# Performance work log

Hardware: AMD Instinct MI355X
Metric: run time of the kernel (lower is better)

Reference implementation:

```python
import jax, jax.numpy as jnp
import numpy as np

NUM_GROUPS = 4
NUM_HEADS = 4
EPS = 1e-6

def group_norm(x, scale, bias):
    # x: [B, C, L]
    b, c, l = x.shape
    g = NUM_GROUPS
    xg = x.reshape(b, g, (c // g) * l)
    mean = xg.mean(axis=-1, keepdims=True)
    var = xg.var(axis=-1, keepdims=True)
    xg = (xg - mean) * jax.lax.rsqrt(var + EPS)
    xn = xg.reshape(b, c, l)
    return xn * scale[None, :, None] + bias[None, :, None]

def conv1x1(x, w, b):
    # x: [B, C_in, L], w: [C_out, C_in], b: [C_out]
    return jnp.einsum('oc,bcl->bol', w, x) + b[None, :, None]

def setup_inputs() -> dict:
    key = jax.random.key(0)
    ks = jax.random.split(key, 11)
    B, C, L = 8, 512, 2048
    x = jax.random.normal(ks[0], (B, C, L), dtype=jnp.float32)
    s = 1.0 / np.sqrt(C)
    return {
        'x': x,
        'gn_scale': jnp.ones((C,), jnp.float32),
        'gn_bias': jnp.zeros((C,), jnp.float32),
        'wq': jax.random.normal(ks[1], (C, C), jnp.float32) * s,
        'bq': jnp.zeros((C,), jnp.float32),
        'wk': jax.random.normal(ks[2], (C, C), jnp.float32) * s,
        'bk': jnp.zeros((C,), jnp.float32),
        'wv': jax.random.normal(ks[3], (C, C), jnp.float32) * s,
        'bv': jnp.zeros((C,), jnp.float32),
        'wo': jax.random.normal(ks[4], (C, C), jnp.float32) * s,
        'bo': jnp.zeros((C,), jnp.float32),
    }

def reference(x, gn_scale, gn_bias, wq, bq, wk, bk, wv, bv, wo, bo):
    b, c, l = x.shape
    nh = NUM_HEADS
    hd = c // nh
    h_ = group_norm(x, gn_scale, gn_bias)
    q = conv1x1(h_, wq, bq).reshape(b, nh, hd, l)
    k = conv1x1(h_, wk, bk).reshape(b, nh, hd, l)
    v = conv1x1(h_, wv, bv).reshape(b, nh, hd, l)
    # scores: [b, nh, l(query), l(key)]
    w_ = jnp.einsum('bhdq,bhdk->bhqk', q, k) * (hd ** -0.5)
    w_ = jax.nn.softmax(w_, axis=-1)
    # attn: [b, nh, l(query), hd]
    attn = jnp.einsum('bhqk,bhdk->bhqd', w_, v)
    attn = attn.transpose(0, 1, 3, 2).reshape(b, c, l)
    out = conv1x1(attn, wo, bo)
    return x + out
```

## Files before the change

kernel.cpp:

```cpp
#include <hip/hip_runtime.h>


typedef unsigned short u16;
typedef unsigned int   u32;
typedef unsigned long long u64;
typedef __attribute__((ext_vector_type(8)))  short          bf16x8;
typedef __attribute__((ext_vector_type(4)))  float          f32x4;
typedef __attribute__((ext_vector_type(16))) float          f32x16;
typedef __attribute__((ext_vector_type(4)))  unsigned int   u32x4;
typedef __attribute__((ext_vector_type(8)))  unsigned short u16x8;

#define MFMA16(a, b, c) __builtin_amdgcn_mfma_f32_16x16x32_bf16((a), (b), (c), 0, 0, 0)
#define MFMA32(a, b, c) __builtin_amdgcn_mfma_f32_32x32x16_bf16((a), (b), (c), 0, 0, 0)

#define WAIT_VM8        16248
#define WAIT_LGKM0      49279
#define BARRIER() __builtin_amdgcn_s_barrier()

__device__ __forceinline__ u16 f2bf(float f) {
    union { float f; unsigned int i; } cv;
    cv.f = f;
    unsigned int u = cv.i;
    u += 0x7fffu + ((u >> 16) & 1);
    return (u16)(u >> 16);
}
__device__ __forceinline__ u32 fbits(float f) {
    union { float f; unsigned int i; } cv; cv.f = f; return cv.i;
}

__device__ __forceinline__ u32 cvtpk_bf16(float lo, float hi) {
    u32 d;
    asm("v_cvt_pk_bf16_f32 %0, %1, %2" : "=v"(d) : "v"(lo), "v"(hi));
    return d;
}
__device__ __forceinline__ void permswap(u32& a, u32& b) {
    asm("v_permlane32_swap_b32 %0, %1" : "+v"(a), "+v"(b));
}

__device__ __forceinline__ void async16(const u16* g, u16* l) {
    __builtin_amdgcn_global_load_lds(
        (const __attribute__((address_space(1))) unsigned int*)g,
        (__attribute__((address_space(3))) unsigned int*)l, 16, 0, 0);
}

#define BATCH 8
#define CCH   512
#define LEN   2048
#define NGRP  4
#define NHEAD 4
#define HD    128
#define GSIZE (128 * 2048)

__global__ __launch_bounds__(256) void prep_k(const float* __restrict__ x,
                                              float* __restrict__ stats,
                                              const float* __restrict__ w0,
                                              const float* __restrict__ w1,
                                              const float* __restrict__ w2,
                                              const float* __restrict__ w3,
                                              u16* __restrict__ dst) {
    const int bid = blockIdx.x;
    if (bid < 256) {
        const int grp   = bid >> 3;
        const int chunk = bid & 7;
        const int b = grp >> 2, g = grp & 3;
        const float* base = x + ((size_t)(b * CCH + g * 128 + chunk * 16)) * LEN;

        float s = 0.f, ss = 0.f;
        for (int i = 0; i < 32; ++i) {
            int cid = threadIdx.x + i * 256;
            f32x4 dv = *(const f32x4*)(base + (size_t)cid * 4);
            for (int u = 0; u < 4; ++u) { s += dv[u]; ss += dv[u] * dv[u]; }
        }
        for (int m = 1; m < 64; m <<= 1) {
            s  += __shfl_xor(s,  m, 64);
            ss += __shfl_xor(ss, m, 64);
        }
        __shared__ float red[8];
        int wid = threadIdx.x >> 6, lane = threadIdx.x & 63;
        if (lane == 0) { red[wid * 2] = s; red[wid * 2 + 1] = ss; }
        __syncthreads();
        if (threadIdx.x == 0) {
            float ts  = red[0] + red[2] + red[4] + red[6];
            float tss = red[1] + red[3] + red[5] + red[7];
            atomicAdd(&stats[grp * 2],     ts);
            atomicAdd(&stats[grp * 2 + 1], tss);
        }
    } else {
        const int wb = bid - 256;
        const int mat = wb >> 7, chunk = wb & 127;
        const float* src = (mat == 0) ? w0 : (mat == 1) ? w1 : (mat == 2) ? w2 : w3;
        const size_t base = (size_t)chunk * 2048 + (size_t)threadIdx.x * 8;
        f32x4 a = *(const f32x4*)(src + base);
        f32x4 b2 = *(const f32x4*)(src + base + 4);
        u16x8 o;
        for (int u = 0; u < 4; ++u) { o[u] = f2bf(a[u]); o[u + 4] = f2bf(b2[u]); }
        *(u16x8*)(dst + (size_t)mat * 262144 + base) = o;
    }
}

__global__ __launch_bounds__(256) void gn_apply_k(const float* __restrict__ x,
                                                  const float* __restrict__ gns,
                                                  const float* __restrict__ gnb,
                                                  const float* __restrict__ stats,
                                                  u16* __restrict__ hT) {
    __shared__ u16 Ts[64 * 72];
    const int b = blockIdx.z, c0 = blockIdx.y * 64, l0 = blockIdx.x * 64;
    const int g = c0 >> 7;
    const int tid = threadIdx.x;

    float sum   = stats[(b * NGRP + g) * 2];
    float sumsq = stats[(b * NGRP + g) * 2 + 1];
    const float invN = 1.f / (float)GSIZE;
    float mean = sum * invN;
    float var  = sumsq * invN - mean * mean;
    float rstd = rsqrtf(var + 1e-6f);

    for (int i = 0; i < 4; ++i) {
        int cid = tid + i * 256;
        int row = cid >> 4, c4 = cid & 15;
        int c = c0 + row;
        float sc = gns[c] * rstd;
        float bi = gnb[c] - mean * sc;
        f32x4 dv = *(const f32x4*)(x + ((size_t)(b * CCH + c)) * LEN + l0 + c4 * 4);
        for (int u = 0; u < 4; ++u)
            Ts[row * 72 + c4 * 4 + u] = f2bf(dv[u] * sc + bi);
    }
    __syncthreads();
    for (int i = 0; i < 2; ++i) {
        int cid = tid + i * 256;
        int lrow = cid >> 3, c8 = cid & 7;
        u16x8 ov;
        for (int u = 0; u < 8; ++u) ov[u] = Ts[(c8 * 8 + u) * 72 + lrow];
        *(u16x8*)(hT + ((size_t)b * LEN + l0 + lrow) * CCH + c0 + c8 * 8) = ov;
    }
}

__global__ __launch_bounds__(256, 2) void gemm01_k(const u16* __restrict__ hT,
                                                   const u16* __restrict__ wq_bf,
                                                   const u16* __restrict__ wk_bf,
                                                   const u16* __restrict__ wv_bf,
                                                   const float* __restrict__ bq,
                                                   const float* __restrict__ bk,
                                                   const float* __restrict__ bv,
                                                   u16* __restrict__ qT,
                                                   u16* __restrict__ kT,
                                                   u16* __restrict__ vbuf) {
    __shared__ u16 As[2][128 * 64];
    __shared__ u16 Bs[2][128 * 64];
    const int bid = blockIdx.x;
    const bool mode0 = (bid < 1024);
    int b, m0, n0;
    const u16 *Arow, *Brow;
    if (mode0) {
        b = bid >> 7; m0 = ((bid >> 3) & 15) * 128; n0 = (bid & 7) * 128;
        Arow = hT + ((size_t)b * LEN + m0) * 512;
        Brow = (n0 < 512) ? (wq_bf + (size_t)n0 * 512)
                          : (wk_bf + (size_t)(n0 - 512) * 512);
    } else {
        int bid2 = bid - 1024;
        b = bid2 >> 6; m0 = ((bid2 >> 4) & 3) * 128; n0 = (bid2 & 15) * 128;
        Arow = wv_bf + (size_t)m0 * 512;
        Brow = hT + ((size_t)b * LEN + n0) * 512;
    }

    const int tid = threadIdx.x;
    const int lane = tid & 63, wid = tid >> 6;
    const int quad = lane >> 4, l15 = lane & 15;
    const int wm = (wid & 1) * 64, wn = (wid >> 1) * 64;

    f32x4 acc[4][4] = {};
    const int srl = lane >> 3, scl = lane & 7;

#pragma unroll
    for (int i = 0; i < 4; ++i) {
        int rloc = wid * 32 + i * 8 + srl;
        int lc = scl ^ (rloc & 7);
        async16(Arow + (size_t)rloc * 512 + lc * 8, &As[0][(wid * 32 + i * 8) * 64]);
        async16(Brow + (size_t)rloc * 512 + lc * 8, &Bs[0][(wid * 32 + i * 8) * 64]);
    }
    __syncthreads();

    for (int kk = 0; kk < 8; ++kk) {
        const int p = kk & 1;
        if (kk < 7) {
            const int k0n = (kk + 1) * 64;
#pragma unroll
            for (int i = 0; i < 4; ++i) {
                int rloc = wid * 32 + i * 8 + srl;
                int lc = scl ^ (rloc & 7);
                async16(Arow + (size_t)rloc * 512 + k0n + lc * 8,
                        &As[1 - p][(wid * 32 + i * 8) * 64]);
                async16(Brow + (size_t)rloc * 512 + k0n + lc * 8,
                        &Bs[1 - p][(wid * 32 + i * 8) * 64]);
            }
        }
#pragma unroll
        for (int ks = 0; ks < 2; ++ks) {
            bf16x8 af[4], bfr[4];
            for (int t = 0; t < 4; ++t) {
                int ra = wm + t * 16 + l15, rb = wn + t * 16 + l15;
                af[t]  = *(const bf16x8*)(&As[p][ra * 64 + (((ks * 4 + quad) ^ (ra & 7))) * 8]);
                bfr[t] = *(const bf16x8*)(&Bs[p][rb * 64 + (((ks * 4 + quad) ^ (rb & 7))) * 8]);
            }
            for (int mt = 0; mt < 4; ++mt)
                for (int nt = 0; nt < 4; ++nt)
                    acc[mt][nt] = MFMA16(af[mt], bfr[nt], acc[mt][nt]);
        }
        __syncthreads();
    }

    if (mode0) {
        const int col0 = (n0 < 512) ? n0 : n0 - 512;
        const float* biasp = ((n0 < 512) ? bq : bk) + col0;
        u16* outp = (n0 < 512) ? qT : kT;
        for (int nt = 0; nt < 4; ++nt) {
            int nl = wn + nt * 16 + l15;
            float bv_ = biasp[nl];
            for (int mt = 0; mt < 4; ++mt)
                for (int r = 0; r < 4; ++r) {
                    int ml = wm + mt * 16 + quad * 4 + r;
                    size_t idx = ((size_t)b * LEN + m0 + ml) * 512 + col0 + nl;
                    outp[idx] = f2bf(acc[mt][nt][r] + bv_);
                }
        }
    } else {
        for (int mt = 0; mt < 4; ++mt)
            for (int r = 0; r < 4; ++r) {
                int ml = wm + mt * 16 + quad * 4 + r;
                float bv_ = bv[m0 + ml];
                for (int nt = 0; nt < 4; ++nt) {
                    int nl = wn + nt * 16 + l15;
                    size_t idx = ((size_t)(b * 512 + m0 + ml)) * LEN + n0 + nl;
                    vbuf[idx] = f2bf(acc[mt][nt][r] + bv_);
                }
            }
    }
}

__global__ __launch_bounds__(256, 2) void gemm2_k(const u16* __restrict__ A0,
                                                  const u16* __restrict__ B0,
                                                  const float* __restrict__ bias0,
                                                  const float* __restrict__ resid,
                                                  float* __restrict__ out0) {
    __shared__ u16 As[2][128 * 64];
    __shared__ u16 Bs[2][128 * 64];
    const int b  = blockIdx.z;
    const int n0 = blockIdx.x * 128;
    const int m0 = blockIdx.y * 128;
    const int tid = threadIdx.x;
    const int lane = tid & 63, wid = tid >> 6;
    const int quad = lane >> 4, l15 = lane & 15;
    const int wm = (wid & 1) * 64, wn = (wid >> 1) * 64;

    const u16* Arow = A0 + (size_t)m0 * 512;
    const u16* Brow = B0 + ((size_t)b * LEN + n0) * 512;

    f32x4 acc[4][4] = {};
    const int srl = lane >> 3, scl = lane & 7;

#pragma unroll
    for (int i = 0; i < 4; ++i) {
        int rloc = wid * 32 + i * 8 + srl;
        int lc = scl ^ (rloc & 7);
        async16(Arow + (size_t)rloc * 512 + lc * 8, &As[0][(wid * 32 + i * 8) * 64]);
        async16(Brow + (size_t)rloc * 512 + lc * 8, &Bs[0][(wid * 32 + i * 8) * 64]);
    }
    __syncthreads();

    for (int kk = 0; kk < 8; ++kk) {
        const int p = kk & 1;
        if (kk < 7) {
            const int k0n = (kk + 1) * 64;
#pragma unroll
            for (int i = 0; i < 4; ++i) {
                int rloc = wid * 32 + i * 8 + srl;
                int lc = scl ^ (rloc & 7);
                async16(Arow + (size_t)rloc * 512 + k0n + lc * 8,
                        &As[1 - p][(wid * 32 + i * 8) * 64]);
                async16(Brow + (size_t)rloc * 512 + k0n + lc * 8,
                        &Bs[1 - p][(wid * 32 + i * 8) * 64]);
            }
        }
#pragma unroll
        for (int ks = 0; ks < 2; ++ks) {
            bf16x8 af[4], bfr[4];
            for (int t = 0; t < 4; ++t) {
                int ra = wm + t * 16 + l15, rb = wn + t * 16 + l15;
                af[t]  = *(const bf16x8*)(&As[p][ra * 64 + (((ks * 4 + quad) ^ (ra & 7))) * 8]);
                bfr[t] = *(const bf16x8*)(&Bs[p][rb * 64 + (((ks * 4 + quad) ^ (rb & 7))) * 8]);
            }
            for (int mt = 0; mt < 4; ++mt)
                for (int nt = 0; nt < 4; ++nt)
                    acc[mt][nt] = MFMA16(af[mt], bfr[nt], acc[mt][nt]);
        }
        __syncthreads();
    }

    for (int mt = 0; mt < 4; ++mt)
        for (int r = 0; r < 4; ++r) {
            int ml = wm + mt * 16 + quad * 4 + r;
            float bv_ = bias0[m0 + ml];
            for (int nt = 0; nt < 4; ++nt) {
                int nl = wn + nt * 16 + l15;
                size_t idx = ((size_t)(b * 512 + m0 + ml)) * LEN + n0 + nl;
                out0[idx] = acc[mt][nt][r] + bv_ + resid[idx];
            }
        }
}

__global__ __launch_bounds__(256, 2) void attn_k(const u16* __restrict__ qT,
                                                 const u16* __restrict__ kT,
                                                 const u16* __restrict__ v,
                                                 u16* __restrict__ attnT) {
    __shared__ u16 Ks[2][64 * 128];
    __shared__ u16 Vs[2][128 * 64];
    const int bid = blockIdx.x;
    const int xcd = bid & 7, slot = bid >> 3;
    const int bh  = xcd * 4 + (slot >> 4);
    const int qt  = slot & 15;
    const int b = bh >> 2, h = bh & 3;
    const int i0 = qt * 128;

    const int tid = threadIdx.x, lane = tid & 63, wg = tid >> 6;
    const int l31 = lane & 31, half = lane >> 5;
    const int mrow = wg * 32 + l31;

    bf16x8 qa[8];
#pragma unroll
    for (int ks = 0; ks < 8; ++ks)
        qa[ks] = *(const bf16x8*)(qT + ((size_t)b * LEN + i0 + mrow) * 512 + h * HD +
                                  ks * 16 + half * 8);

    float mst = -3.0e38f, lst = 0.f;
    f32x16 oacc[4] = {};

    const float SL2E = 0.08838834764831845f * 1.4426950408889634f;

    const u16* kbase = kT + ((size_t)b * LEN) * 512 + h * HD;
    const u16* vbase = v + ((size_t)(b * CCH + h * HD)) * LEN;
    const u16* kgp[4];
    const u16* vgp[4];
    int krow[4], vrow[4];
#pragma unroll
    for (int i = 0; i < 4; ++i) {
        int rk = wg * 16 + i * 4 + (lane >> 4);
        krow[i] = wg * 16 + i * 4;
        kgp[i] = kbase + (size_t)rk * 512 + ((lane & 15) ^ (rk & 7)) * 8;
        int rv = wg * 32 + i * 8 + (lane >> 3);
        vrow[i] = wg * 32 + i * 8;
        vgp[i] = vbase + (size_t)rv * LEN + ((lane & 7) ^ (rv & 7)) * 8;
    }

#pragma unroll
    for (int i = 0; i < 4; ++i) {
        async16(kgp[i], &Ks[0][krow[i] * 128]);
        async16(vgp[i], &Vs[0][vrow[i] * 64]);
        kgp[i] += 64 * 512;
        vgp[i] += 64;
    }

    for (int jt = 0; jt < 32; ++jt) {
        const int p = jt & 1;

#pragma unroll
        for (int i = 0; i < 4; ++i) async16(kgp[i], &Ks[1 - p][krow[i] * 128]);
#pragma unroll
        for (int i = 0; i < 4; ++i) async16(vgp[i], &Vs[1 - p][vrow[i] * 64]);
        if (jt < 30) {
#pragma unroll
            for (int i = 0; i < 4; ++i) { kgp[i] += 64 * 512; vgp[i] += 64; }
        }

        __builtin_amdgcn_s_waitcnt(WAIT_VM8);
        BARRIER();

        f32x16 st[2] = {};
#pragma unroll
        for (int t = 0; t < 2; ++t) {
            int r = t * 32 + l31;
#pragma unroll
            for (int ks = 0; ks < 8; ++ks) {
                bf16x8 kf = *(const bf16x8*)(&Ks[p][r * 128 + ((ks * 2 + half) ^ (r & 7)) * 8]);
                st[t] = MFMA32(kf, qa[ks], st[t]);
            }
        }

        float rm = -3.0e38f;
#pragma unroll
        for (int t = 0; t < 2; ++t)
            for (int r = 0; r < 16; ++r) rm = fmaxf(rm, st[t][r]);
        rm *= SL2E;
        rm = fmaxf(rm, __shfl_xor(rm, 32, 64));
        float mnew  = fmaxf(mst, rm);
        float alpha = __builtin_amdgcn_exp2f(mst - mnew);
        mst = mnew;
        float rs = 0.f;
#pragma unroll
        for (int t = 0; t < 2; ++t)
            for (int r = 0; r < 16; ++r) {
                float pv_ = __builtin_amdgcn_exp2f(st[t][r] * SL2E - mnew);
                st[t][r] = pv_;
                rs += pv_;
            }
        rs += __shfl_xor(rs, 32, 64);
        lst = lst * alpha + rs;
        if (__ballot(alpha != 1.0f) != 0ull) {
#pragma unroll
            for (int dt = 0; dt < 4; ++dt)
                for (int r = 0; r < 16; ++r) oacc[dt][r] *= alpha;
        }

        u32 pw[4][4];
#pragma unroll
        for (int t = 0; t < 2; ++t) {
            u32 Ag[4], Bg[4];
#pragma unroll
            for (int g = 0; g < 4; ++g) {
                Ag[g] = cvtpk_bf16(st[t][g * 4 + 0], st[t][g * 4 + 1]);
                Bg[g] = cvtpk_bf16(st[t][g * 4 + 2], st[t][g * 4 + 3]);
            }
#pragma unroll
            for (int u = 0; u < 2; ++u) {
                u32 a0 = Ag[2 * u], a1 = Ag[2 * u + 1];
                u32 b0 = Bg[2 * u], b1 = Bg[2 * u + 1];
                permswap(a0, a1);
                permswap(b0, b1);
                const int jb = t * 2 + u;
                pw[jb][0] = a0; pw[jb][1] = b0; pw[jb][2] = a1; pw[jb][3] = b1;
            }
        }

#pragma unroll
        for (int jb = 0; jb < 4; ++jb) {
            union { u32 w[4]; bf16x8 v8; } pu_;
            pu_.w[0] = pw[jb][0]; pu_.w[1] = pw[jb][1];
            pu_.w[2] = pw[jb][2]; pu_.w[3] = pw[jb][3];
#pragma unroll
            for (int dt = 0; dt < 4; ++dt) {
                int d = dt * 32 + l31;
                bf16x8 vf = *(const bf16x8*)(&Vs[p][d * 64 + ((jb * 2 + half) ^ (d & 7)) * 8]);
                oacc[dt] = MFMA32(vf, pu_.v8, oacc[dt]);
            }
        }

        __builtin_amdgcn_s_waitcnt(WAIT_LGKM0);
        BARRIER();
    }

    float inv = 1.f / lst;
    for (int dt = 0; dt < 4; ++dt)
        for (int g = 0; g < 4; ++g) {
            u64 w =  (u64)f2bf(oacc[dt][g * 4 + 0] * inv)
                  | ((u64)f2bf(oacc[dt][g * 4 + 1] * inv) << 16)
                  | ((u64)f2bf(oacc[dt][g * 4 + 2] * inv) << 32)
                  | ((u64)f2bf(oacc[dt][g * 4 + 3] * inv) << 48);
            int c = h * HD + dt * 32 + g * 8 + half * 4;
            *(u64*)(attnT + ((size_t)b * LEN + i0 + mrow) * 512 + c) = w;
        }
}

extern "C" void kernel_launch(void* const* d_in, const int* in_sizes, int n_in,
                              void* d_out, int out_size, void* d_ws, size_t ws_size,
                              hipStream_t stream) {
    const float* x   = (const float*)d_in[0];
    const float* gns = (const float*)d_in[1];
    const float* gnb = (const float*)d_in[2];
    const float* wq  = (const float*)d_in[3];
    const float* bq  = (const float*)d_in[4];
    const float* wk  = (const float*)d_in[5];
    const float* bk  = (const float*)d_in[6];
    const float* wv  = (const float*)d_in[7];
    const float* bv  = (const float*)d_in[8];
    const float* wo  = (const float*)d_in[9];
    const float* bo  = (const float*)d_in[10];
    float* out = (float*)d_out;

    const size_t NEL = (size_t)BATCH * CCH * LEN;
    float* stats = (float*)d_ws;
    u16* wcat  = (u16*)((char*)d_ws + 256);
    u16* hT    = wcat + 4 * 262144;
    u16* qT    = hT + NEL;
    u16* kT    = qT + NEL;
    u16* vbuf  = kT + NEL;
    u16* attnT = hT;

    const u16* wq_bf = wcat;
    const u16* wk_bf = wcat + 262144;
    const u16* wv_bf = wcat + 2 * 262144;
    const u16* wo_bf = wcat + 3 * 262144;

    hipMemsetAsync(d_ws, 0, 256, stream);
    prep_k<<<768, 256, 0, stream>>>(x, stats, wq, wk, wv, wo, wcat);
    gn_apply_k<<<dim3(32, 8, 8), 256, 0, stream>>>(x, gns, gnb, stats, hT);
    gemm01_k<<<1536, 256, 0, stream>>>(hT, wq_bf, wk_bf, wv_bf, bq, bk, bv, qT, kT, vbuf);
    attn_k<<<512, 256, 0, stream>>>(qT, kT, vbuf, attnT);
    gemm2_k<<<dim3(16, 4, 8), 256, 0, stream>>>(wo_bf, attnT, bo, x, out);
}
```

Baseline: 254.0 us.

## Software-pipeline QK^T of next tile with softmax/PV of current tile in attention

Restructures the attention main loop so the QK^T MFMA for tile j+1 is issued before the softmax and PV work for tile j, using ping-pong score registers and a macro unrolled by two. K and V loads are split and staggered so the V buffer is refilled only after its PV use. The change also adds s_setprio around the compute section and tree reductions for the row max and row sum. The goal is to overlap MFMA with the exp/VALU work and shorten the dependency chain, at the cost of extra live registers for the second score tile, which risks spills at the 2-blocks-per-CU launch bound.

```diff
diff --git a/kernel.cpp b/kernel.cpp
--- a/kernel.cpp
+++ b/kernel.cpp
@@ -14,6 +14,7 @@
 #define MFMA32(a, b, c) __builtin_amdgcn_mfma_f32_32x32x16_bf16((a), (b), (c), 0, 0, 0)
 
 #define WAIT_VM8        16248
+#define WAIT_VM4        16244
 #define WAIT_LGKM0      49279
 #define BARRIER() __builtin_amdgcn_s_barrier()
 
@@ -27,6 +28,7 @@
 __device__ __forceinline__ u32 fbits(float f) {
     union { float f; unsigned int i; } cv; cv.f = f; return cv.i;
 }
+__device__ __forceinline__ f32x16 fzero16() { f32x16 z = {}; return z; }
 
 __device__ __forceinline__ u32 cvtpk_bf16(float lo, float hi) {
     u32 d;
@@ -308,6 +310,112 @@
         }
 }
 
+#define ATTN_STAGE(JT, P, STO, STN)                                            \
+  {                                                                            \
+    _Pragma("unroll")                                                          \
+    for (int i = 0; i < 4; ++i) async16(kgp[i], &Ks[P][krow[i] * 128]);        \
+    if ((JT) < 29) {                                                           \
+      _Pragma("unroll")                                                        \
+      for (int i = 0; i < 4; ++i) kgp[i] += 64 * 512;                          \
+    }                                                                          \
+    __builtin_amdgcn_s_waitcnt(WAIT_VM8);                                      \
+    BARRIER();                                                                 \
+    __builtin_amdgcn_s_setprio(1);                                             \
+    if ((JT) < 31) {                                                           \
+      STN[0] = fzero16(); STN[1] = fzero16();                                  \
+      _Pragma("unroll")                                                        \
+      for (int t = 0; t < 2; ++t) {                                            \
+        int r = t * 32 + l31;                                                  \
+        _Pragma("unroll")                                                      \
+        for (int ks = 0; ks < 8; ++ks) {                                       \
+          bf16x8 kf = *(const bf16x8*)(&Ks[1 - (P)][r * 128 +                  \
+                          ((ks * 2 + half) ^ (r & 7)) * 8]);                   \
+          STN[t] = MFMA32(kf, qa[ks], STN[t]);                                 \
+        }                                                                      \
+      }                                                                        \
+    }                                                                          \
+         \
+    float rm;                                                                  \
+    {                                                                          \
+      float t0[8];                                                             \
+      _Pragma("unroll")                                                        \
+      for (int r = 0; r < 8; ++r)                                              \
+        t0[r] = fmaxf(fmaxf(STO[0][r], STO[0][r + 8]),                         \
+                      fmaxf(STO[1][r], STO[1][r + 8]));                        \
+      float a0 = fmaxf(t0[0], t0[1]), a1 = fmaxf(t0[2], t0[3]);                \
+      float a2 = fmaxf(t0[4], t0[5]), a3 = fmaxf(t0[6], t0[7]);                \
+      rm = fmaxf(fmaxf(a0, a1), fmaxf(a2, a3));                                \
+    }                                                                          \
+    rm *= SL2E;                                                                \
+    rm = fmaxf(rm, __shfl_xor(rm, 32, 64));                                    \
+    float mnew  = fmaxf(mst, rm);                                              \
+    float alpha = __builtin_amdgcn_exp2f(mst - mnew);                          \
+    mst = mnew;                                                                \
+    _Pragma("unroll")                                                          \
+    for (int t = 0; t < 2; ++t)                                                \
+      for (int r = 0; r < 16; ++r)                                             \
+        STO[t][r] = __builtin_amdgcn_exp2f(STO[t][r] * SL2E - mnew);           \
+    float rs;                                                                  \
+    {                                                                          \
+      float s0[8];                                                             \
+      _Pragma("unroll")                                                        \
+      for (int r = 0; r < 8; ++r)                                              \
+        s0[r] = (STO[0][r] + STO[0][r + 8]) + (STO[1][r] + STO[1][r + 8]);     \
+      float b0 = s0[0] + s0[1], b1 = s0[2] + s0[3];                            \
+      float b2 = s0[4] + s0[5], b3 = s0[6] + s0[7];                            \
+      rs = (b0 + b1) + (b2 + b3);                                              \
+    }                                                                          \
+    rs += __shfl_xor(rs, 32, 64);                                              \
+    lst = lst * alpha + rs;                                                    \
+    if (__ballot(alpha != 1.0f) != 0ull) {                                     \
+      _Pragma("unroll")                                                        \
+      for (int dt = 0; dt < 4; ++dt)                                           \
+        for (int r = 0; r < 16; ++r) oacc[dt][r] *= alpha;                     \
+    }                                                                          \
+                               \
+    u32 pw[4][4];                                                              \
+    _Pragma("unroll")                                                          \
+    for (int t = 0; t < 2; ++t) {                                              \
+      u32 Ag[4], Bg[4];                                                        \
+      _Pragma("unroll")                                                        \
+      for (int g = 0; g < 4; ++g) {                                            \
+        Ag[g] = cvtpk_bf16(STO[t][g * 4 + 0], STO[t][g * 4 + 1]);              \
+        Bg[g] = cvtpk_bf16(STO[t][g * 4 + 2], STO[t][g * 4 + 3]);              \
+      }                                                                        \
+      _Pragma("unroll")                                                        \
+      for (int u = 0; u < 2; ++u) {                                            \
+        u32 a0 = Ag[2 * u], a1 = Ag[2 * u + 1];                                \
+        u32 b0 = Bg[2 * u], b1 = Bg[2 * u + 1];                                \
+        permswap(a0, a1); permswap(b0, b1);                                    \
+        const int jb = t * 2 + u;                                              \
+        pw[jb][0] = a0; pw[jb][1] = b0; pw[jb][2] = a1; pw[jb][3] = b1;        \
+      }                                                                        \
+    }                                                                          \
+                              \
+    _Pragma("unroll")                                                          \
+    for (int jb = 0; jb < 4; ++jb) {                                           \
+      union { u32 w[4]; bf16x8 v8; } pu_;                                      \
+      pu_.w[0] = pw[jb][0]; pu_.w[1] = pw[jb][1];                              \
+      pu_.w[2] = pw[jb][2]; pu_.w[3] = pw[jb][3];                              \
+      _Pragma("unroll")                                                        \
+      for (int dt = 0; dt < 4; ++dt) {                                         \
+        int d = dt * 32 + l31;                                                 \
+        bf16x8 vf = *(const bf16x8*)(&Vs[P][d * 64 +                           \
+                        ((jb * 2 + half) ^ (d & 7)) * 8]);                     \
+        oacc[dt] = MFMA32(vf, pu_.v8, oacc[dt]);                               \
+      }                                                                        \
+    }                                                                          \
+    __builtin_amdgcn_s_setprio(0);                                             \
+    __builtin_amdgcn_s_waitcnt(WAIT_LGKM0);                                    \
+    BARRIER();                                                                 \
+    _Pragma("unroll")                                                          \
+    for (int i = 0; i < 4; ++i) async16(vgp[i], &Vs[P][vrow[i] * 64]);         \
+    if ((JT) < 29) {                                                           \
+      _Pragma("unroll")                                                        \
+      for (int i = 0; i < 4; ++i) vgp[i] += 64;                                \
+    }                                                                          \
+  }
+
 __global__ __launch_bounds__(256, 2) void attn_k(const u16* __restrict__ qT,
                                                  const u16* __restrict__ kT,
                                                  const u16* __restrict__ v,
@@ -355,96 +463,37 @@
     for (int i = 0; i < 4; ++i) {
         async16(kgp[i], &Ks[0][krow[i] * 128]);
         async16(vgp[i], &Vs[0][vrow[i] * 64]);
-        kgp[i] += 64 * 512;
-        vgp[i] += 64;
-    }
-
-    for (int jt = 0; jt < 32; ++jt) {
-        const int p = jt & 1;
-
-#pragma unroll
-        for (int i = 0; i < 4; ++i) async16(kgp[i], &Ks[1 - p][krow[i] * 128]);
-#pragma unroll
-        for (int i = 0; i < 4; ++i) async16(vgp[i], &Vs[1 - p][vrow[i] * 64]);
-        if (jt < 30) {
-#pragma unroll
-            for (int i = 0; i < 4; ++i) { kgp[i] += 64 * 512; vgp[i] += 64; }
-        }
-
-        __builtin_amdgcn_s_waitcnt(WAIT_VM8);
-        BARRIER();
-
-        f32x16 st[2] = {};
-#pragma unroll
-        for (int t = 0; t < 2; ++t) {
-            int r = t * 32 + l31;
-#pragma unroll
-            for (int ks = 0; ks < 8; ++ks) {
-                bf16x8 kf = *(const bf16x8*)(&Ks[p][r * 128 + ((ks * 2 + half) ^ (r & 7)) * 8]);
-                st[t] = MFMA32(kf, qa[ks], st[t]);
-            }
-        }
-
-        float rm = -3.0e38f;
-#pragma unroll
-        for (int t = 0; t < 2; ++t)
-            for (int r = 0; r < 16; ++r) rm = fmaxf(rm, st[t][r]);
-        rm *= SL2E;
-        rm = fmaxf(rm, __shfl_xor(rm, 32, 64));
-        float mnew  = fmaxf(mst, rm);
-        float alpha = __builtin_amdgcn_exp2f(mst - mnew);
-        mst = mnew;
-        float rs = 0.f;
-#pragma unroll
-        for (int t = 0; t < 2; ++t)
-            for (int r = 0; r < 16; ++r) {
-                float pv_ = __builtin_amdgcn_exp2f(st[t][r] * SL2E - mnew);
-                st[t][r] = pv_;
-                rs += pv_;
-            }
-        rs += __shfl_xor(rs, 32, 64);
-        lst = lst * alpha + rs;
-        if (__ballot(alpha != 1.0f) != 0ull) {
-#pragma unroll
-            for (int dt = 0; dt < 4; ++dt)
-                for (int r = 0; r < 16; ++r) oacc[dt][r] *= alpha;
-        }
-
-        u32 pw[4][4];
-#pragma unroll
-        for (int t = 0; t < 2; ++t) {
-            u32 Ag[4], Bg[4];
-#pragma unroll
-            for (int g = 0; g < 4; ++g) {
-                Ag[g] = cvtpk_bf16(st[t][g * 4 + 0], st[t][g * 4 + 1]);
-                Bg[g] = cvtpk_bf16(st[t][g * 4 + 2], st[t][g * 4 + 3]);
-            }
-#pragma unroll
-            for (int u = 0; u < 2; ++u) {
-                u32 a0 = Ag[2 * u], a1 = Ag[2 * u + 1];
-                u32 b0 = Bg[2 * u], b1 = Bg[2 * u + 1];
-                permswap(a0, a1);
-                permswap(b0, b1);
-                const int jb = t * 2 + u;
-                pw[jb][0] = a0; pw[jb][1] = b0; pw[jb][2] = a1; pw[jb][3] = b1;
-            }
-        }
-
-#pragma unroll
-        for (int jb = 0; jb < 4; ++jb) {
-            union { u32 w[4]; bf16x8 v8; } pu_;
-            pu_.w[0] = pw[jb][0]; pu_.w[1] = pw[jb][1];
-            pu_.w[2] = pw[jb][2]; pu_.w[3] = pw[jb][3];
-#pragma unroll
-            for (int dt = 0; dt < 4; ++dt) {
-                int d = dt * 32 + l31;
-                bf16x8 vf = *(const bf16x8*)(&Vs[p][d * 64 + ((jb * 2 + half) ^ (d & 7)) * 8]);
-                oacc[dt] = MFMA32(vf, pu_.v8, oacc[dt]);
-            }
-        }
-
-        __builtin_amdgcn_s_waitcnt(WAIT_LGKM0);
-        BARRIER();
+    }
+#pragma unroll
+    for (int i = 0; i < 4; ++i) { kgp[i] += 64 * 512; vgp[i] += 64; }
+#pragma unroll
+    for (int i = 0; i < 4; ++i) async16(kgp[i], &Ks[1][krow[i] * 128]);
+#pragma unroll
+    for (int i = 0; i < 4; ++i) kgp[i] += 64 * 512;
+
+    __builtin_amdgcn_s_waitcnt(WAIT_VM4);
+    BARRIER();
+
+#pragma unroll
+    for (int i = 0; i < 4; ++i) async16(vgp[i], &Vs[1][vrow[i] * 64]);
+#pragma unroll
+    for (int i = 0; i < 4; ++i) vgp[i] += 64;
+
+    f32x16 stA[2], stB[2];
+    stA[0] = fzero16(); stA[1] = fzero16();
+#pragma unroll
+    for (int t = 0; t < 2; ++t) {
+        int r = t * 32 + l31;
+#pragma unroll
+        for (int ks = 0; ks < 8; ++ks) {
+            bf16x8 kf = *(const bf16x8*)(&Ks[0][r * 128 + ((ks * 2 + half) ^ (r & 7)) * 8]);
+            stA[t] = MFMA32(kf, qa[ks], stA[t]);
+        }
+    }
+
+    for (int jt = 0; jt < 32; jt += 2) {
+        ATTN_STAGE(jt,     0, stA, stB);
+        ATTN_STAGE(jt + 1, 1, stB, stA);
     }
 
     float inv = 1.f / lst;
```

Result: no change. 256.0 us (+0.8%).

## Split attention key range across two wave groups and fold softmax scale into Q

Applied to the files above, without the earlier changes.

The attention kernel now runs 512 threads per block. Two groups of four waves each process half of a 128-key tile, and their flash-attention partial states (max, sum, output) are merged through shared memory at the end. The softmax scale times log2(e) is folded into Q when the QKV GEMM writes it, which removes a per-element multiply in the attention loop. The change also adds tree reductions for row max and sum and s_setprio around the compute. In exchange it doubles LDS per block to 128 KB, which likely allows only one block per CU, and adds an end-of-kernel merge step.

```diff
diff --git a/kernel.cpp b/kernel.cpp
--- a/kernel.cpp
+++ b/kernel.cpp
@@ -14,8 +14,11 @@
 #define MFMA32(a, b, c) __builtin_amdgcn_mfma_f32_32x32x16_bf16((a), (b), (c), 0, 0, 0)
 
 #define WAIT_VM8        16248
+#define WAIT_VM0        16240
 #define WAIT_LGKM0      49279
 #define BARRIER() __builtin_amdgcn_s_barrier()
+
+#define SL2E 0.12754316089246708f
 
 __device__ __forceinline__ u16 f2bf(float f) {
     union { float f; unsigned int i; } cv;
@@ -210,9 +213,11 @@
     }
 
     if (mode0) {
-        const int col0 = (n0 < 512) ? n0 : n0 - 512;
-        const float* biasp = ((n0 < 512) ? bq : bk) + col0;
-        u16* outp = (n0 < 512) ? qT : kT;
+        const bool isq = (n0 < 512);
+        const int col0 = isq ? n0 : n0 - 512;
+        const float* biasp = (isq ? bq : bk) + col0;
+        u16* outp = isq ? qT : kT;
+        const float osc = isq ? SL2E : 1.0f;
         for (int nt = 0; nt < 4; ++nt) {
             int nl = wn + nt * 16 + l15;
             float bv_ = biasp[nl];
@@ -220,7 +225,7 @@
                 for (int r = 0; r < 4; ++r) {
                     int ml = wm + mt * 16 + quad * 4 + r;
                     size_t idx = ((size_t)b * LEN + m0 + ml) * 512 + col0 + nl;
-                    outp[idx] = f2bf(acc[mt][nt][r] + bv_);
+                    outp[idx] = f2bf((acc[mt][nt][r] + bv_) * osc);
                 }
         }
     } else {
@@ -308,12 +313,12 @@
         }
 }
 
-__global__ __launch_bounds__(256, 2) void attn_k(const u16* __restrict__ qT,
+__global__ __launch_bounds__(512, 2) void attn_k(const u16* __restrict__ qT,
                                                  const u16* __restrict__ kT,
                                                  const u16* __restrict__ v,
                                                  u16* __restrict__ attnT) {
-    __shared__ u16 Ks[2][64 * 128];
-    __shared__ u16 Vs[2][128 * 64];
+    __shared__ u16 Ks[2][128 * 128];
+    __shared__ u16 Vs[2][128 * 128];
     const int bid = blockIdx.x;
     const int xcd = bid & 7, slot = bid >> 3;
     const int bh  = xcd * 4 + (slot >> 4);
@@ -323,7 +328,8 @@
 
     const int tid = threadIdx.x, lane = tid & 63, wg = tid >> 6;
     const int l31 = lane & 31, half = lane >> 5;
-    const int mrow = wg * 32 + l31;
+    const int mi = wg & 3, ji = wg >> 2;
+    const int mrow = mi * 32 + l31;
 
     bf16x8 qa[8];
 #pragma unroll
@@ -333,75 +339,91 @@
 
     float mst = -3.0e38f, lst = 0.f;
     f32x16 oacc[4] = {};
-
-    const float SL2E = 0.08838834764831845f * 1.4426950408889634f;
+    const f32x16 FZ = {};
 
     const u16* kbase = kT + ((size_t)b * LEN) * 512 + h * HD;
     const u16* vbase = v + ((size_t)(b * CCH + h * HD)) * LEN;
     const u16* kgp[4];
     const u16* vgp[4];
-    int krow[4], vrow[4];
+    int wrow[4];
 #pragma unroll
     for (int i = 0; i < 4; ++i) {
-        int rk = wg * 16 + i * 4 + (lane >> 4);
-        krow[i] = wg * 16 + i * 4;
-        kgp[i] = kbase + (size_t)rk * 512 + ((lane & 15) ^ (rk & 7)) * 8;
-        int rv = wg * 32 + i * 8 + (lane >> 3);
-        vrow[i] = wg * 32 + i * 8;
-        vgp[i] = vbase + (size_t)rv * LEN + ((lane & 7) ^ (rv & 7)) * 8;
+        int r = wg * 16 + i * 4 + (lane >> 4);
+        wrow[i] = wg * 16 + i * 4;
+        kgp[i] = kbase + (size_t)r * 512 + ((lane & 15) ^ (r & 7)) * 8;
+        vgp[i] = vbase + (size_t)r * LEN + ((lane & 15) ^ (r & 7)) * 8;
     }
 
 #pragma unroll
     for (int i = 0; i < 4; ++i) {
-        async16(kgp[i], &Ks[0][krow[i] * 128]);
-        async16(vgp[i], &Vs[0][vrow[i] * 64]);
-        kgp[i] += 64 * 512;
-        vgp[i] += 64;
-    }
-
-    for (int jt = 0; jt < 32; ++jt) {
-        const int p = jt & 1;
-
-#pragma unroll
-        for (int i = 0; i < 4; ++i) async16(kgp[i], &Ks[1 - p][krow[i] * 128]);
-#pragma unroll
-        for (int i = 0; i < 4; ++i) async16(vgp[i], &Vs[1 - p][vrow[i] * 64]);
-        if (jt < 30) {
-#pragma unroll
-            for (int i = 0; i < 4; ++i) { kgp[i] += 64 * 512; vgp[i] += 64; }
+        async16(kgp[i], &Ks[0][wrow[i] * 128]);
+        async16(vgp[i], &Vs[0][wrow[i] * 128]);
+        kgp[i] += 128 * 512;
+        vgp[i] += 128;
+    }
+
+    for (int t = 0; t < 16; ++t) {
+        const int p = t & 1;
+
+#pragma unroll
+        for (int i = 0; i < 4; ++i) async16(kgp[i], &Ks[1 - p][wrow[i] * 128]);
+#pragma unroll
+        for (int i = 0; i < 4; ++i) async16(vgp[i], &Vs[1 - p][wrow[i] * 128]);
+        if (t < 14) {
+#pragma unroll
+            for (int i = 0; i < 4; ++i) { kgp[i] += 128 * 512; vgp[i] += 128; }
         }
 
         __builtin_amdgcn_s_waitcnt(WAIT_VM8);
         BARRIER();
-
-        f32x16 st[2] = {};
-#pragma unroll
-        for (int t = 0; t < 2; ++t) {
-            int r = t * 32 + l31;
-#pragma unroll
-            for (int ks = 0; ks < 8; ++ks) {
-                bf16x8 kf = *(const bf16x8*)(&Ks[p][r * 128 + ((ks * 2 + half) ^ (r & 7)) * 8]);
-                st[t] = MFMA32(kf, qa[ks], st[t]);
-            }
-        }
-
-        float rm = -3.0e38f;
-#pragma unroll
-        for (int t = 0; t < 2; ++t)
-            for (int r = 0; r < 16; ++r) rm = fmaxf(rm, st[t][r]);
-        rm *= SL2E;
+        __builtin_amdgcn_s_setprio(1);
+
+        f32x16 st[2];
+#pragma unroll
+        for (int tt = 0; tt < 2; ++tt) {
+            int r = ji * 64 + tt * 32 + l31;
+            {
+                int u0 = ((0 * 2 + half) & 7) ^ (r & 7);
+                bf16x8 kf = *(const bf16x8*)(&Ks[p][r * 128 + u0 * 8]);
+                st[tt] = MFMA32(kf, qa[0], FZ);
+            }
+#pragma unroll
+            for (int ks = 1; ks < 8; ++ks) {
+                int u = ((ks & 4) << 1) | (((ks * 2 + half) & 7) ^ (r & 7));
+                bf16x8 kf = *(const bf16x8*)(&Ks[p][r * 128 + u * 8]);
+                st[tt] = MFMA32(kf, qa[ks], st[tt]);
+            }
+        }
+
+        float rm;
+        {
+            float t0[8];
+#pragma unroll
+            for (int r = 0; r < 8; ++r)
+                t0[r] = fmaxf(fmaxf(st[0][r], st[0][r + 8]),
+                              fmaxf(st[1][r], st[1][r + 8]));
+            float a0 = fmaxf(t0[0], t0[1]), a1 = fmaxf(t0[2], t0[3]);
+            float a2 = fmaxf(t0[4], t0[5]), a3 = fmaxf(t0[6], t0[7]);
+            rm = fmaxf(fmaxf(a0, a1), fmaxf(a2, a3));
+        }
         rm = fmaxf(rm, __shfl_xor(rm, 32, 64));
         float mnew  = fmaxf(mst, rm);
         float alpha = __builtin_amdgcn_exp2f(mst - mnew);
         mst = mnew;
-        float rs = 0.f;
-#pragma unroll
-        for (int t = 0; t < 2; ++t)
-            for (int r = 0; r < 16; ++r) {
-                float pv_ = __builtin_amdgcn_exp2f(st[t][r] * SL2E - mnew);
-                st[t][r] = pv_;
-                rs += pv_;
-            }
+#pragma unroll
+        for (int tt = 0; tt < 2; ++tt)
+            for (int r = 0; r < 16; ++r)
+                st[tt][r] = __builtin_amdgcn_exp2f(st[tt][r] - mnew);
+        float rs;
+        {
+            float s0[8];
+#pragma unroll
+            for (int r = 0; r < 8; ++r)
+                s0[r] = (st[0][r] + st[0][r + 8]) + (st[1][r] + st[1][r + 8]);
+            float b0 = s0[0] + s0[1], b1 = s0[2] + s0[3];
+            float b2 = s0[4] + s0[5], b3 = s0[6] + s0[7];
+            rs = (b0 + b1) + (b2 + b3);
+        }
         rs += __shfl_xor(rs, 32, 64);
         lst = lst * alpha + rs;
         if (__ballot(alpha != 1.0f) != 0ull) {
@@ -412,20 +434,19 @@
 
         u32 pw[4][4];
 #pragma unroll
-        for (int t = 0; t < 2; ++t) {
+        for (int tt = 0; tt < 2; ++tt) {
             u32 Ag[4], Bg[4];
 #pragma unroll
             for (int g = 0; g < 4; ++g) {
-                Ag[g] = cvtpk_bf16(st[t][g * 4 + 0], st[t][g * 4 + 1]);
-                Bg[g] = cvtpk_bf16(st[t][g * 4 + 2], st[t][g * 4 + 3]);
+                Ag[g] = cvtpk_bf16(st[tt][g * 4 + 0], st[tt][g * 4 + 1]);
+                Bg[g] = cvtpk_bf16(st[tt][g * 4 + 2], st[tt][g * 4 + 3]);
             }
 #pragma unroll
             for (int u = 0; u < 2; ++u) {
                 u32 a0 = Ag[2 * u], a1 = Ag[2 * u + 1];
                 u32 b0 = Bg[2 * u], b1 = Bg[2 * u + 1];
-                permswap(a0, a1);
-                permswap(b0, b1);
-                const int jb = t * 2 + u;
+                permswap(a0, a1); permswap(b0, b1);
+                const int jb = tt * 2 + u;
                 pw[jb][0] = a0; pw[jb][1] = b0; pw[jb][2] = a1; pw[jb][3] = b1;
             }
         }
@@ -438,25 +459,74 @@
 #pragma unroll
             for (int dt = 0; dt < 4; ++dt) {
                 int d = dt * 32 + l31;
-                bf16x8 vf = *(const bf16x8*)(&Vs[p][d * 64 + ((jb * 2 + half) ^ (d & 7)) * 8]);
+                int u = ji * 8 + (((jb * 2 + half)) ^ (d & 7));
+                bf16x8 vf = *(const bf16x8*)(&Vs[p][d * 128 + u * 8]);
                 oacc[dt] = MFMA32(vf, pu_.v8, oacc[dt]);
             }
         }
 
+        __builtin_amdgcn_s_setprio(0);
         __builtin_amdgcn_s_waitcnt(WAIT_LGKM0);
         BARRIER();
     }
 
-    float inv = 1.f / lst;
+    __builtin_amdgcn_s_waitcnt(WAIT_VM0);
+    BARRIER();
+
+    float* MLb = (float*)&Ks[0][0];
+    if (half == 0) {
+        MLb[wg * 64 + l31]      = mst;
+        MLb[wg * 64 + 32 + l31] = lst;
+    }
+    BARRIER();
+
+    const int pw_ = wg ^ 4;
+    float m_p = MLb[pw_ * 64 + l31];
+    float l_p = MLb[pw_ * 64 + 32 + l31];
+    float Mn  = fmaxf(mst, m_p);
+    float bs  = __builtin_amdgcn_exp2f(mst - Mn);
+    float bp  = __builtin_amdgcn_exp2f(m_p - Mn);
+    float ltot = bs * lst + bp * l_p;
+#pragma unroll
     for (int dt = 0; dt < 4; ++dt)
-        for (int g = 0; g < 4; ++g) {
-            u64 w =  (u64)f2bf(oacc[dt][g * 4 + 0] * inv)
-                  | ((u64)f2bf(oacc[dt][g * 4 + 1] * inv) << 16)
-                  | ((u64)f2bf(oacc[dt][g * 4 + 2] * inv) << 32)
-                  | ((u64)f2bf(oacc[dt][g * 4 + 3] * inv) << 48);
-            int c = h * HD + dt * 32 + g * 8 + half * 4;
-            *(u64*)(attnT + ((size_t)b * LEN + i0 + mrow) * 512 + c) = w;
-        }
+        for (int r = 0; r < 16; ++r) oacc[dt][r] *= bs;
+
+    float* Ob = (mi < 2) ? (float*)&Ks[1][0] : (float*)&Vs[1][0];
+    const int obase = (mi & 1) * 4096;
+    if (ji == 1) {
+#pragma unroll
+        for (int dt = 0; dt < 4; ++dt)
+            for (int g = 0; g < 4; ++g) {
+                int cidx = dt * 8 + g * 2 + half;
+                int cs = (cidx & 24) | ((cidx & 7) ^ (l31 & 7));
+                f32x4 tv;
+                tv[0] = oacc[dt][g * 4 + 0]; tv[1] = oacc[dt][g * 4 + 1];
+                tv[2] = oacc[dt][g * 4 + 2]; tv[3] = oacc[dt][g * 4 + 3];
+                *(f32x4*)&Ob[obase + l31 * 128 + cs * 4] = tv;
+            }
+    }
+    BARRIER();
+
+    if (ji == 0) {
+        float inv = 1.f / ltot;
+#pragma unroll
+        for (int dt = 0; dt < 4; ++dt)
+            for (int g = 0; g < 4; ++g) {
+                int cidx = dt * 8 + g * 2 + half;
+                int cs = (cidx & 24) | ((cidx & 7) ^ (l31 & 7));
+                f32x4 rd = *(const f32x4*)&Ob[obase + l31 * 128 + cs * 4];
+                float o0 = (oacc[dt][g * 4 + 0] + rd[0]) * inv;
+                float o1 = (oacc[dt][g * 4 + 1] + rd[1]) * inv;
+                float o2 = (oacc[dt][g * 4 + 2] + rd[2]) * inv;
+                float o3 = (oacc[dt][g * 4 + 3] + rd[3]) * inv;
+                u64 w =  (u64)f2bf(o0)
+                      | ((u64)f2bf(o1) << 16)
+                      | ((u64)f2bf(o2) << 32)
+                      | ((u64)f2bf(o3) << 48);
+                int c = h * HD + dt * 32 + g * 8 + half * 4;
+                *(u64*)(attnT + ((size_t)b * LEN + i0 + mrow) * 512 + c) = w;
+            }
+    }
 }
 
 extern "C" void kernel_launch(void* const* d_in, const int* in_sizes, int n_in,
@@ -493,6 +563,6 @@
     prep_k<<<768, 256, 0, stream>>>(x, stats, wq, wk, wv, wo, wcat);
     gn_apply_k<<<dim3(32, 8, 8), 256, 0, stream>>>(x, gns, gnb, stats, hT);
     gemm01_k<<<1536, 256, 0, stream>>>(hT, wq_bf, wk_bf, wv_bf, bq, bk, bv, qT, kT, vbuf);
-    attn_k<<<512, 256, 0, stream>>>(qT, kT, vbuf, attnT);
+    attn_k<<<512, 512, 0, stream>>>(qT, kT, vbuf, attnT);
     gemm2_k<<<dim3(16, 4, 8), 256, 0, stream>>>(wo_bf, attnT, bo, x, out);
 }
```

Result: slower. 270.6 us (+6.5%).
